# Kernel optimization log

Hardware: AMD Instinct MI355X
Metric: run time of the kernel (lower is better)

Reference implementation:

```python
import jax, jax.numpy as jnp
import numpy as np

T, H = 4096, 2048


def setup_inputs() -> dict:
    key = jax.random.key(0)
    k_a, k_b, k_x = jax.random.split(key, 3)
    # glorot-style init matching the module: uniform(-1,1) * sqrt(2/sum(shape))
    a = jax.random.uniform(k_a, (H,), minval=-1.0, maxval=1.0) * jnp.sqrt(2.0 / H)
    B = jax.random.uniform(k_b, (H, H), minval=-1.0, maxval=1.0) * jnp.sqrt(2.0 / (2 * H))
    x = jax.random.normal(k_x, (T, H), dtype=jnp.float32)
    return {"x": x, "a": a, "B": B}


def reference(x, a, B):
    # x: (T, H); per-timestep s_t = B.T @ x_t  ->  s = x @ B, laid out NCH = (1, H, T)
    Tl, Hl = x.shape
    s = jnp.einsum("th,hk->kt", x, B)[None]  # (1, H, T)
    # depthwise causal kernel: k[h, t] = a[h]**t, time as final dim, flipped for conv
    exponents = jnp.arange(Tl)
    kernel = jnp.power(a[:, None], exponents)          # (H, T)
    kernel_flipped = jnp.flip(kernel, axis=-1)[:, None, :]  # (H, 1, T) OIH
    s_padded = jnp.pad(s, ((0, 0), (0, 0), (Tl - 1, 0)))    # causal left-pad
    conv_out = jax.lax.conv_general_dilated(
        s_padded, kernel_flipped,
        window_strides=(1,), padding="VALID",
        dimension_numbers=("NCH", "OIH", "NCH"),
        feature_group_count=Hl,
    )  # (1, H, T): h_t[h] = sum_{k<=t} a[h]**(t-k) * s_k[h]
    return jnp.transpose(conv_out, (0, 2, 1))  # (1, T, H)
```

## Files before the change

### kernel.cpp

```cpp
#include <hip/hip_runtime.h>
#include <stdint.h>

#define TDIM 4096
#define HDIM 2048

#define BM 128
#define BN 128
#define BK 32

typedef short short8 __attribute__((ext_vector_type(8)));
typedef float f32x4 __attribute__((ext_vector_type(4)));

__device__ __forceinline__ uint16_t f2bf(float f) {
  uint32_t u = __builtin_bit_cast(uint32_t, f);
  u += 0x7fffu + ((u >> 16) & 1u);
  return (uint16_t)(u >> 16);
}
__device__ __forceinline__ float bf2f(uint16_t h) {
  uint32_t u = ((uint32_t)h) << 16;
  return __builtin_bit_cast(float, u);
}

__device__ __forceinline__ void async_copy16(const void* gsrc, void* ldst) {
  __builtin_amdgcn_global_load_lds(
      (const __attribute__((address_space(1))) uint32_t*)gsrc,
      (__attribute__((address_space(3))) uint32_t*)ldst,
      16, 0, 0);
}

__global__ void cvt_x(const float* __restrict__ in, uint16_t* __restrict__ out) {
  size_t i = ((size_t)blockIdx.x * 256 + threadIdx.x) * 8;
  float4 v0 = *(const float4*)(in + i);
  float4 v1 = *(const float4*)(in + i + 4);
  union { uint16_t h[8]; uint4 v; } o;
  o.h[0] = f2bf(v0.x); o.h[1] = f2bf(v0.y); o.h[2] = f2bf(v0.z); o.h[3] = f2bf(v0.w);
  o.h[4] = f2bf(v1.x); o.h[5] = f2bf(v1.y); o.h[6] = f2bf(v1.z); o.h[7] = f2bf(v1.w);
  *(uint4*)(out + i) = o.v;
}

__global__ void transpose_cvt(const float* __restrict__ B, uint16_t* __restrict__ Bt) {
  __shared__ uint16_t tile[64][65];
  const int k0 = blockIdx.y * 64;
  const int n0 = blockIdx.x * 64;
  const int tid = threadIdx.x;
  for (int i = 0; i < 16; ++i) {
    int idx = i * 256 + tid;
    int r = idx >> 6, c = idx & 63;
    tile[r][c] = f2bf(B[(size_t)(k0 + r) * HDIM + n0 + c]);
  }
  __syncthreads();
  for (int i = 0; i < 16; ++i) {
    int idx = i * 256 + tid;
    int r = idx >> 6, c = idx & 63;
    Bt[(size_t)(n0 + r) * HDIM + k0 + c] = tile[c][r];
  }
}

__global__ __launch_bounds__(256) void gemm_bf16(
    const uint16_t* __restrict__ A, const uint16_t* __restrict__ Bt,
    uint16_t* __restrict__ S) {
  __shared__ __align__(16) uint16_t As[BM * BK];
  __shared__ __align__(16) uint16_t Bs[BN * BK];

  const int tid  = threadIdx.x;
  const int lane = tid & 63;
  const int wave = tid >> 6;
  const int wm = (wave >> 1) * 64;
  const int wn = (wave & 1) * 64;
  const int m0 = blockIdx.y * BM;
  const int n0 = blockIdx.x * BN;

  f32x4 acc[4][4] = {};

  const int srow = wave * 16 + (lane >> 2);
  const int scol = (lane & 3) * 16;
  const char* aptr = (const char*)A + ((size_t)(m0 + srow) * HDIM) * 2 + scol;
  const char* bptr = (const char*)Bt + ((size_t)(n0 + srow) * HDIM) * 2 + scol;
  char* As_base = (char*)As + wave * 1024;
  char* Bs_base = (char*)Bs + wave * 1024;
  const size_t rowskip = (size_t)64 * HDIM * 2;

  const int fr = lane & 15;
  const int fq = lane >> 4;

  for (int kt = 0; kt < HDIM / BK; ++kt) {
    __syncthreads();
    async_copy16(aptr,           As_base);
    async_copy16(aptr + rowskip, As_base + 4096);
    async_copy16(bptr,           Bs_base);
    async_copy16(bptr + rowskip, Bs_base + 4096);
    aptr += BK * 2;
    bptr += BK * 2;
    asm volatile("s_waitcnt vmcnt(0)" ::: "memory");
    __syncthreads();

    short8 af[4], bfr[4];
#pragma unroll
    for (int im = 0; im < 4; ++im)
      af[im] = *(const short8*)&As[(wm + im * 16 + fr) * BK + fq * 8];
#pragma unroll
    for (int in = 0; in < 4; ++in)
      bfr[in] = *(const short8*)&Bs[(wn + in * 16 + fr) * BK + fq * 8];
#pragma unroll
    for (int im = 0; im < 4; ++im)
#pragma unroll
      for (int in = 0; in < 4; ++in)
        acc[im][in] = __builtin_amdgcn_mfma_f32_16x16x32_bf16(
            af[im], bfr[in], acc[im][in], 0, 0, 0);
  }

#pragma unroll
  for (int im = 0; im < 4; ++im) {
#pragma unroll
    for (int in = 0; in < 4; ++in) {
      int col  = n0 + wn + in * 16 + fr;
      int rowb = m0 + wm + im * 16 + fq * 4;
#pragma unroll
      for (int r = 0; r < 4; ++r)
        S[(size_t)(rowb + r) * HDIM + col] = f2bf(acc[im][in][r]);
    }
  }
}

#define TT 64
#define WARM 16
__global__ void conv_scan(const uint16_t* __restrict__ S, const float* __restrict__ a,
                          float* __restrict__ out) {
  const int h  = blockIdx.x * 256 + threadIdx.x;
  const int t0 = blockIdx.y * TT;
  const float av = a[h];
  float acc = 0.f;
  int tstart = t0 - WARM;
  if (tstart < 0) tstart = 0;
  for (int t = tstart; t < t0 + TT; ++t) {
    float s = bf2f(S[(size_t)t * HDIM + h]);
    acc = av * acc + s;
    if (t >= t0) out[(size_t)t * HDIM + h] = acc;
  }
}

extern "C" void kernel_launch(void* const* d_in, const int* in_sizes, int n_in,
                              void* d_out, int out_size, void* d_ws, size_t ws_size,
                              hipStream_t stream) {
  const float* x = (const float*)d_in[0];
  const float* a = (const float*)d_in[1];
  const float* B = (const float*)d_in[2];
  float* out = (float*)d_out;

  uint16_t* xb  = (uint16_t*)d_ws;
  uint16_t* Btb = (uint16_t*)((char*)d_ws + (size_t)16 * 1024 * 1024);
  uint16_t* S   = (uint16_t*)((char*)d_ws + (size_t)24 * 1024 * 1024);

  cvt_x<<<(TDIM * HDIM) / (8 * 256), 256, 0, stream>>>(x, xb);
  transpose_cvt<<<dim3(HDIM / 64, HDIM / 64), 256, 0, stream>>>(B, Btb);
  gemm_bf16<<<dim3(HDIM / BN, TDIM / BM), 256, 0, stream>>>(xb, Btb, S);
  conv_scan<<<dim3(HDIM / 256, TDIM / TT), 256, 0, stream>>>(S, a, out);
}
```

Measured before the change: 165.5 us.

## Swizzle GEMM LDS, use 8 waves per block, vectorize conv scan over channels

The GEMM block is reorganized to 512 threads with each wave computing a 64x32 tile, and an XOR swizzle is added to the LDS chunk layout so fragment reads avoid bank conflicts. The scan kernel now processes four channels per thread with vector loads and stores, fully unrolled, and uses shorter time tiles. The shorter tiles increase the warmup re-read of S relative to useful work, trading extra reads for more parallelism and wider memory accesses.

```diff
diff --git a/kernel.cpp b/kernel.cpp
--- a/kernel.cpp
+++ b/kernel.cpp
@@ -16,8 +16,8 @@
   u += 0x7fffu + ((u >> 16) & 1u);
   return (uint16_t)(u >> 16);
 }
-__device__ __forceinline__ float bf2f(uint16_t h) {
-  uint32_t u = ((uint32_t)h) << 16;
+__device__ __forceinline__ float bf2f(uint32_t h) {
+  uint32_t u = h << 16;
   return __builtin_bit_cast(float, u);
 }
 
@@ -56,7 +56,7 @@
   }
 }
 
-__global__ __launch_bounds__(256) void gemm_bf16(
+__global__ __launch_bounds__(512) void gemm_bf16(
     const uint16_t* __restrict__ A, const uint16_t* __restrict__ Bt,
     uint16_t* __restrict__ S) {
   __shared__ __align__(16) uint16_t As[BM * BK];
@@ -65,46 +65,48 @@
   const int tid  = threadIdx.x;
   const int lane = tid & 63;
   const int wave = tid >> 6;
-  const int wm = (wave >> 1) * 64;
-  const int wn = (wave & 1) * 64;
+  const int wm = (wave >> 2) * 64;
+  const int wn = (wave & 3) * 32;
   const int m0 = blockIdx.y * BM;
   const int n0 = blockIdx.x * BN;
 
-  f32x4 acc[4][4] = {};
+  f32x4 acc[4][2] = {};
 
-  const int srow = wave * 16 + (lane >> 2);
-  const int scol = (lane & 3) * 16;
-  const char* aptr = (const char*)A + ((size_t)(m0 + srow) * HDIM) * 2 + scol;
-  const char* bptr = (const char*)Bt + ((size_t)(n0 + srow) * HDIM) * 2 + scol;
+  const int rloc  = lane >> 2;
+  const int swzl  = (rloc & 3) ^ ((rloc >> 2) & 3);
+  const int gchunk = (lane & 3) ^ swzl;
+  const char* aptr = (const char*)A +
+      ((size_t)(m0 + wave * 16 + rloc) * HDIM + gchunk * 8) * 2;
+  const char* bptr = (const char*)Bt +
+      ((size_t)(n0 + wave * 16 + rloc) * HDIM + gchunk * 8) * 2;
   char* As_base = (char*)As + wave * 1024;
   char* Bs_base = (char*)Bs + wave * 1024;
-  const size_t rowskip = (size_t)64 * HDIM * 2;
 
   const int fr = lane & 15;
   const int fq = lane >> 4;
+  const int swzf = (fr & 3) ^ ((fr >> 2) & 3);
+  const int rchunk = fq ^ swzf;
 
   for (int kt = 0; kt < HDIM / BK; ++kt) {
     __syncthreads();
-    async_copy16(aptr,           As_base);
-    async_copy16(aptr + rowskip, As_base + 4096);
-    async_copy16(bptr,           Bs_base);
-    async_copy16(bptr + rowskip, Bs_base + 4096);
+    async_copy16(aptr, As_base);
+    async_copy16(bptr, Bs_base);
     aptr += BK * 2;
     bptr += BK * 2;
     asm volatile("s_waitcnt vmcnt(0)" ::: "memory");
     __syncthreads();
 
-    short8 af[4], bfr[4];
+    short8 af[4], bfr[2];
 #pragma unroll
     for (int im = 0; im < 4; ++im)
-      af[im] = *(const short8*)&As[(wm + im * 16 + fr) * BK + fq * 8];
+      af[im] = *(const short8*)&As[(wm + im * 16 + fr) * BK + rchunk * 8];
 #pragma unroll
-    for (int in = 0; in < 4; ++in)
-      bfr[in] = *(const short8*)&Bs[(wn + in * 16 + fr) * BK + fq * 8];
+    for (int in = 0; in < 2; ++in)
+      bfr[in] = *(const short8*)&Bs[(wn + in * 16 + fr) * BK + rchunk * 8];
 #pragma unroll
     for (int im = 0; im < 4; ++im)
 #pragma unroll
-      for (int in = 0; in < 4; ++in)
+      for (int in = 0; in < 2; ++in)
         acc[im][in] = __builtin_amdgcn_mfma_f32_16x16x32_bf16(
             af[im], bfr[in], acc[im][in], 0, 0, 0);
   }
@@ -112,7 +114,7 @@
 #pragma unroll
   for (int im = 0; im < 4; ++im) {
 #pragma unroll
-    for (int in = 0; in < 4; ++in) {
+    for (int in = 0; in < 2; ++in) {
       int col  = n0 + wn + in * 16 + fr;
       int rowb = m0 + wm + im * 16 + fq * 4;
 #pragma unroll
@@ -122,20 +124,35 @@
   }
 }
 
-#define TT 64
+#define TT 16
 #define WARM 16
 __global__ void conv_scan(const uint16_t* __restrict__ S, const float* __restrict__ a,
                           float* __restrict__ out) {
-  const int h  = blockIdx.x * 256 + threadIdx.x;
+  const int h  = (blockIdx.x * 256 + threadIdx.x) * 4;
   const int t0 = blockIdx.y * TT;
-  const float av = a[h];
-  float acc = 0.f;
-  int tstart = t0 - WARM;
-  if (tstart < 0) tstart = 0;
-  for (int t = tstart; t < t0 + TT; ++t) {
-    float s = bf2f(S[(size_t)t * HDIM + h]);
-    acc = av * acc + s;
-    if (t >= t0) out[(size_t)t * HDIM + h] = acc;
+  const float4 av = *(const float4*)(a + h);
+  float a0 = 0.f, a1 = 0.f, a2 = 0.f, a3 = 0.f;
+  if (t0 > 0) {
+#pragma unroll
+    for (int i = 0; i < WARM; ++i) {
+      int t = t0 - WARM + i;
+      uint2 sv = *(const uint2*)(S + (size_t)t * HDIM + h);
+      a0 = av.x * a0 + bf2f(sv.x & 0xffffu);
+      a1 = av.y * a1 + bf2f(sv.x >> 16);
+      a2 = av.z * a2 + bf2f(sv.y & 0xffffu);
+      a3 = av.w * a3 + bf2f(sv.y >> 16);
+    }
+  }
+#pragma unroll
+  for (int i = 0; i < TT; ++i) {
+    int t = t0 + i;
+    uint2 sv = *(const uint2*)(S + (size_t)t * HDIM + h);
+    a0 = av.x * a0 + bf2f(sv.x & 0xffffu);
+    a1 = av.y * a1 + bf2f(sv.x >> 16);
+    a2 = av.z * a2 + bf2f(sv.y & 0xffffu);
+    a3 = av.w * a3 + bf2f(sv.y >> 16);
+    float4 o = make_float4(a0, a1, a2, a3);
+    *(float4*)(out + (size_t)t * HDIM + h) = o;
   }
 }
 
@@ -153,6 +170,6 @@
 
   cvt_x<<<(TDIM * HDIM) / (8 * 256), 256, 0, stream>>>(x, xb);
   transpose_cvt<<<dim3(HDIM / 64, HDIM / 64), 256, 0, stream>>>(B, Btb);
-  gemm_bf16<<<dim3(HDIM / BN, TDIM / BM), 256, 0, stream>>>(xb, Btb, S);
-  conv_scan<<<dim3(HDIM / 256, TDIM / TT), 256, 0, stream>>>(S, a, out);
+  gemm_bf16<<<dim3(HDIM / BN, TDIM / BM), 512, 0, stream>>>(xb, Btb, S);
+  conv_scan<<<dim3(HDIM / (256 * 4), TDIM / TT), 256, 0, stream>>>(S, a, out);
 }
```

Result: faster. 152.2 us (-8.0%).
